# Kernel optimization log

Measured on AMD Instinct MI355X. Metric: run time of the kernel, lower is better.

Reference implementation:

```python
import jax, jax.numpy as jnp
import numpy as np

EPS = 1e-16


def _grads4(x):
    """Four directional shift-differences with zero 'same' padding.

    Matches the fixed 3x3 depthwise conv kernels (cross-correlation):
      Gy: x[i-1,j]   - x[i+1,j]
      Gx: x[i,j-1]   - x[i,j+1]
      GD: x[i-1,j-1] - x[i+1,j+1]
      Gd: x[i-1,j+1] - x[i+1,j-1]
    x: [B, C, H, W]
    """
    B, C, H, W = x.shape
    xp = jnp.pad(x, ((0, 0), (0, 0), (1, 1), (1, 1)))  # zero pad like padding='same'
    gy = xp[:, :, 0:H,     1:W + 1] - xp[:, :, 2:H + 2, 1:W + 1]
    gx = xp[:, :, 1:H + 1, 0:W]     - xp[:, :, 1:H + 1, 2:W + 2]
    gD = xp[:, :, 0:H,     0:W]     - xp[:, :, 2:H + 2, 2:W + 2]
    gd = xp[:, :, 0:H,     2:W + 2] - xp[:, :, 2:H + 2, 0:W]
    return jnp.concatenate([gy, gx, gD, gd], axis=1)  # [B, 4C, H, W]


def setup_inputs() -> dict:
    key = jax.random.key(0)
    k1, k2 = jax.random.split(key)
    shape = (16, 6, 512, 512)
    outputs = jax.random.normal(k1, shape, dtype=jnp.float32)
    labels = jax.random.normal(k2, shape, dtype=jnp.float32)
    return {"outputs": outputs, "labels": labels}


def reference(outputs, labels):
    g_out = _grads4(outputs)
    g_lab = _grads4(labels)
    l1 = jnp.mean(jnp.abs(g_out - g_lab))
    return jnp.sqrt(l1 + EPS)
```

## Files before the change

### kernel.cpp

```cpp
#include <hip/hip_runtime.h>
#include <math.h>


#define NTHREADS 256
#define TROWS 16
#define SROWS (TROWS + 2)
#define WV 512
#define HT 512
#define PLANES 96
#define STRIPS (HT / TROWS)
#define NBLOCKS (PLANES * STRIPS)
#define F4_PER_TILE (SROWS * WV / 4)
#define LD_PER_THREAD (F4_PER_TILE / NTHREADS)

struct Row { float d[8]; float eL, eR; };

__device__ __forceinline__ Row lds_row(const float* __restrict__ sd,
                                       int sr, int lane) {
    Row row;
    const float4 a = *reinterpret_cast<const float4*>(sd + sr * WV + lane * 8);
    const float4 b = *reinterpret_cast<const float4*>(sd + sr * WV + lane * 8 + 4);
    row.d[0] = a.x; row.d[1] = a.y; row.d[2] = a.z; row.d[3] = a.w;
    row.d[4] = b.x; row.d[5] = b.y; row.d[6] = b.z; row.d[7] = b.w;
    const float up = __shfl_up(row.d[7], 1, 64);
    const float dn = __shfl_down(row.d[0], 1, 64);
    row.eL = (lane == 0)  ? 0.f : up;
    row.eR = (lane == 63) ? 0.f : dn;
    return row;
}

__global__ __launch_bounds__(NTHREADS, 4) void struct_loss_partial(
        const float* __restrict__ out_p, const float* __restrict__ lab_p,
        float* __restrict__ partials) {
    __shared__ float sd[SROWS * WV];

    const int plane = blockIdx.x >> 5;
    const int strip = blockIdx.x & (STRIPS - 1);
    const int row0  = strip * TROWS;
    const size_t pbase = (size_t)plane * (HT * WV);

    float4 ov[LD_PER_THREAD], lv[LD_PER_THREAD];
    #pragma unroll
    for (int k = 0; k < LD_PER_THREAD; ++k) {
        const int p  = threadIdx.x + NTHREADS * k;
        const int r  = p >> 7;
        const int c4 = p & 127;
        const int gr = row0 + r - 1;
        const int grc = min(max(gr, 0), HT - 1);
        const size_t goff = pbase + (size_t)grc * WV + c4 * 4;
        ov[k] = *reinterpret_cast<const float4*>(out_p + goff);
        lv[k] = *reinterpret_cast<const float4*>(lab_p + goff);
    }
    #pragma unroll
    for (int k = 0; k < LD_PER_THREAD; ++k) {
        const int p = threadIdx.x + NTHREADS * k;
        const int r = p >> 7;
        const int gr = row0 + r - 1;
        const float m = (gr >= 0 && gr < HT) ? 1.f : 0.f;
        float4 d;
        d.x = m * (ov[k].x - lv[k].x);
        d.y = m * (ov[k].y - lv[k].y);
        d.z = m * (ov[k].z - lv[k].z);
        d.w = m * (ov[k].w - lv[k].w);
        *reinterpret_cast<float4*>(sd + (size_t)p * 4) = d;
    }
    __syncthreads();

    const int wv   = threadIdx.x >> 6;
    const int lane = threadIdx.x & 63;
    float acc = 0.f;

    Row rp = lds_row(sd, wv * 4,     lane);
    Row rc = lds_row(sd, wv * 4 + 1, lane);
    #pragma unroll
    for (int rr = 0; rr < 4; ++rr) {
        Row rn = lds_row(sd, wv * 4 + 2 + rr, lane);

        #pragma unroll
        for (int k = 0; k < 8; ++k) {
            const float cL = (k > 0) ? rc.d[k - 1] : rc.eL;
            const float cR = (k < 7) ? rc.d[k + 1] : rc.eR;
            const float pL = (k > 0) ? rp.d[k - 1] : rp.eL;
            const float pR = (k < 7) ? rp.d[k + 1] : rp.eR;
            const float nL = (k > 0) ? rn.d[k - 1] : rn.eL;
            const float nR = (k < 7) ? rn.d[k + 1] : rn.eR;

            const float gy = rp.d[k] - rn.d[k];
            const float gx = cL - cR;
            const float gD = pL - nR;
            const float gd = pR - nL;
            acc += fabsf(gy) + fabsf(gx) + fabsf(gD) + fabsf(gd);
        }
        rp = rc;
        rc = rn;
    }

    #pragma unroll
    for (int off = 32; off > 0; off >>= 1)
        acc += __shfl_down(acc, off, 64);

    __shared__ float smem[NTHREADS / 64];
    if (lane == 0) smem[wv] = acc;
    __syncthreads();
    if (threadIdx.x == 0) {
        float s = 0.f;
        #pragma unroll
        for (int w = 0; w < NTHREADS / 64; ++w) s += smem[w];
        partials[blockIdx.x] = s;
    }
}

__global__ __launch_bounds__(256) void struct_loss_final(
        const float* __restrict__ partial, float* __restrict__ out,
        int nparts, double inv_count) {
    double acc = 0.0;
    for (int i = threadIdx.x; i < nparts; i += blockDim.x)
        acc += (double)partial[i];
    #pragma unroll
    for (int off = 32; off > 0; off >>= 1)
        acc += __shfl_down(acc, off, 64);
    __shared__ double smem[4];
    const int lane = threadIdx.x & 63;
    const int wid  = threadIdx.x >> 6;
    if (lane == 0) smem[wid] = acc;
    __syncthreads();
    if (threadIdx.x == 0) {
        double s = smem[0] + smem[1] + smem[2] + smem[3];
        out[0] = (float)sqrt(s * inv_count + 1e-16);
    }
}

extern "C" void kernel_launch(void* const* d_in, const int* in_sizes, int n_in,
                              void* d_out, int out_size, void* d_ws, size_t ws_size,
                              hipStream_t stream) {
    const float* outputs = (const float*)d_in[0];
    const float* labels  = (const float*)d_in[1];
    float* out = (float*)d_out;
    float* partials = (float*)d_ws;

    const double inv_count = 1.0 / (16.0 * 24.0 * 512.0 * 512.0);

    struct_loss_partial<<<NBLOCKS, NTHREADS, 0, stream>>>(outputs, labels, partials);
    struct_loss_final<<<1, 256, 0, stream>>>(partials, out, NBLOCKS, inv_count);
}
```

Baseline: 42.17 us.

## Load tiles directly into LDS with global_load_lds and halve strip height

Replaces register-staged global loads with direct global-to-LDS DMA loads of both the outputs and labels tiles. The difference and boundary masking now happen at LDS read time instead of before the store. Strip height drops from 16 to 8 rows, doubling the block count, and the occupancy hint in launch bounds is removed. The intent is to cut VGPR pressure and raise memory-level parallelism, at the cost of more halo re-reads (10/8 instead of 18/16) and twice the LDS footprint per block.

```diff
diff --git a/kernel.cpp b/kernel.cpp
--- a/kernel.cpp
+++ b/kernel.cpp
@@ -3,25 +3,36 @@
 
 
 #define NTHREADS 256
-#define TROWS 16
+#define TROWS 8
 #define SROWS (TROWS + 2)
 #define WV 512
 #define HT 512
 #define PLANES 96
 #define STRIPS (HT / TROWS)
 #define NBLOCKS (PLANES * STRIPS)
-#define F4_PER_TILE (SROWS * WV / 4)
-#define LD_PER_THREAD (F4_PER_TILE / NTHREADS)
+#define TILE_F (SROWS * WV)
+#define CHUNKS (2 * SROWS * 2)
+#define CHUNKS_PER_WAVE (CHUNKS / 4)
+
+__device__ __forceinline__ void gload_lds16(const float* g, float* l) {
+    __builtin_amdgcn_global_load_lds(
+        (const __attribute__((address_space(1))) void*)g,
+        (__attribute__((address_space(3))) void*)l, 16, 0, 0);
+}
 
 struct Row { float d[8]; float eL, eR; };
 
 __device__ __forceinline__ Row lds_row(const float* __restrict__ sd,
-                                       int sr, int lane) {
+                                       int sr, int lane, float m) {
+    const float4 a  = *reinterpret_cast<const float4*>(sd + sr * WV + lane * 8);
+    const float4 b  = *reinterpret_cast<const float4*>(sd + sr * WV + lane * 8 + 4);
+    const float4 c  = *reinterpret_cast<const float4*>(sd + TILE_F + sr * WV + lane * 8);
+    const float4 dd = *reinterpret_cast<const float4*>(sd + TILE_F + sr * WV + lane * 8 + 4);
     Row row;
-    const float4 a = *reinterpret_cast<const float4*>(sd + sr * WV + lane * 8);
-    const float4 b = *reinterpret_cast<const float4*>(sd + sr * WV + lane * 8 + 4);
-    row.d[0] = a.x; row.d[1] = a.y; row.d[2] = a.z; row.d[3] = a.w;
-    row.d[4] = b.x; row.d[5] = b.y; row.d[6] = b.z; row.d[7] = b.w;
+    row.d[0] = m * (a.x - c.x);  row.d[1] = m * (a.y - c.y);
+    row.d[2] = m * (a.z - c.z);  row.d[3] = m * (a.w - c.w);
+    row.d[4] = m * (b.x - dd.x); row.d[5] = m * (b.y - dd.y);
+    row.d[6] = m * (b.z - dd.z); row.d[7] = m * (b.w - dd.w);
     const float up = __shfl_up(row.d[7], 1, 64);
     const float dn = __shfl_down(row.d[0], 1, 64);
     row.eL = (lane == 0)  ? 0.f : up;
@@ -29,70 +40,63 @@
     return row;
 }
 
-__global__ __launch_bounds__(NTHREADS, 4) void struct_loss_partial(
+__global__ __launch_bounds__(NTHREADS) void struct_loss_partial(
         const float* __restrict__ out_p, const float* __restrict__ lab_p,
         float* __restrict__ partials) {
-    __shared__ float sd[SROWS * WV];
+    __shared__ float sd[2 * TILE_F];
 
-    const int plane = blockIdx.x >> 5;
+    const int plane = blockIdx.x >> 6;
     const int strip = blockIdx.x & (STRIPS - 1);
     const int row0  = strip * TROWS;
     const size_t pbase = (size_t)plane * (HT * WV);
 
-    float4 ov[LD_PER_THREAD], lv[LD_PER_THREAD];
+    const int wid  = threadIdx.x >> 6;
+    const int lane = threadIdx.x & 63;
+
     #pragma unroll
-    for (int k = 0; k < LD_PER_THREAD; ++k) {
-        const int p  = threadIdx.x + NTHREADS * k;
-        const int r  = p >> 7;
-        const int c4 = p & 127;
-        const int gr = row0 + r - 1;
-        const int grc = min(max(gr, 0), HT - 1);
-        const size_t goff = pbase + (size_t)grc * WV + c4 * 4;
-        ov[k] = *reinterpret_cast<const float4*>(out_p + goff);
-        lv[k] = *reinterpret_cast<const float4*>(lab_p + goff);
-    }
-    #pragma unroll
-    for (int k = 0; k < LD_PER_THREAD; ++k) {
-        const int p = threadIdx.x + NTHREADS * k;
-        const int r = p >> 7;
-        const int gr = row0 + r - 1;
-        const float m = (gr >= 0 && gr < HT) ? 1.f : 0.f;
-        float4 d;
-        d.x = m * (ov[k].x - lv[k].x);
-        d.y = m * (ov[k].y - lv[k].y);
-        d.z = m * (ov[k].z - lv[k].z);
-        d.w = m * (ov[k].w - lv[k].w);
-        *reinterpret_cast<float4*>(sd + (size_t)p * 4) = d;
+    for (int k = 0; k < CHUNKS_PER_WAVE; ++k) {
+        const int c   = wid * CHUNKS_PER_WAVE + k;
+        const int arr = (c >= CHUNKS / 2) ? 1 : 0;
+        const int cc  = c - (CHUNKS / 2) * arr;
+        const int r   = cc >> 1;
+        const int h   = cc & 1;
+        const int gr  = min(max(row0 + r - 1, 0), HT - 1);
+        const float* src = (arr ? lab_p : out_p) + pbase
+                         + (size_t)gr * WV + h * 256 + lane * 4;
+        gload_lds16(src, sd + c * 256);
     }
     __syncthreads();
 
-    const int wv   = threadIdx.x >> 6;
-    const int lane = threadIdx.x & 63;
     float acc = 0.f;
+    {
+        const int sr0 = wid * 2;
+        const float m0 = ((unsigned)(row0 + sr0 - 1) < (unsigned)HT) ? 1.f : 0.f;
+        Row rp = lds_row(sd, sr0,     lane, m0);
+        Row rc = lds_row(sd, sr0 + 1, lane, 1.f);
+        #pragma unroll
+        for (int rr = 0; rr < 2; ++rr) {
+            const int sr = sr0 + 2 + rr;
+            const float mn = ((unsigned)(row0 + sr - 1) < (unsigned)HT) ? 1.f : 0.f;
+            Row rn = lds_row(sd, sr, lane, mn);
 
-    Row rp = lds_row(sd, wv * 4,     lane);
-    Row rc = lds_row(sd, wv * 4 + 1, lane);
-    #pragma unroll
-    for (int rr = 0; rr < 4; ++rr) {
-        Row rn = lds_row(sd, wv * 4 + 2 + rr, lane);
+            #pragma unroll
+            for (int k = 0; k < 8; ++k) {
+                const float cL = (k > 0) ? rc.d[k - 1] : rc.eL;
+                const float cR = (k < 7) ? rc.d[k + 1] : rc.eR;
+                const float pL = (k > 0) ? rp.d[k - 1] : rp.eL;
+                const float pR = (k < 7) ? rp.d[k + 1] : rp.eR;
+                const float nL = (k > 0) ? rn.d[k - 1] : rn.eL;
+                const float nR = (k < 7) ? rn.d[k + 1] : rn.eR;
 
-        #pragma unroll
-        for (int k = 0; k < 8; ++k) {
-            const float cL = (k > 0) ? rc.d[k - 1] : rc.eL;
-            const float cR = (k < 7) ? rc.d[k + 1] : rc.eR;
-            const float pL = (k > 0) ? rp.d[k - 1] : rp.eL;
-            const float pR = (k < 7) ? rp.d[k + 1] : rp.eR;
-            const float nL = (k > 0) ? rn.d[k - 1] : rn.eL;
-            const float nR = (k < 7) ? rn.d[k + 1] : rn.eR;
-
-            const float gy = rp.d[k] - rn.d[k];
-            const float gx = cL - cR;
-            const float gD = pL - nR;
-            const float gd = pR - nL;
-            acc += fabsf(gy) + fabsf(gx) + fabsf(gD) + fabsf(gd);
+                const float gy = rp.d[k] - rn.d[k];
+                const float gx = cL - cR;
+                const float gD = pL - nR;
+                const float gd = pR - nL;
+                acc += fabsf(gy) + fabsf(gx) + fabsf(gD) + fabsf(gd);
+            }
+            rp = rc;
+            rc = rn;
         }
-        rp = rc;
-        rc = rn;
     }
 
     #pragma unroll
@@ -100,7 +104,7 @@
         acc += __shfl_down(acc, off, 64);
 
     __shared__ float smem[NTHREADS / 64];
-    if (lane == 0) smem[wv] = acc;
+    if (lane == 0) smem[wid] = acc;
     __syncthreads();
     if (threadIdx.x == 0) {
         float s = 0.f;
```

After: 48.10 us. 1.14x slower.

## Process four strips per block with register-prefetched next tile overlapping compute

Applied to the files above, without the earlier changes.

Each block now handles four consecutive strips instead of one, cutting the grid by a factor of four. Global loads for the next strip are issued into registers before the current strip's LDS stencil compute, then written to shared memory after a barrier, so load latency overlaps compute. Sched barriers keep the compiler from sinking the loads, and the occupancy hint in launch bounds is dropped. The trade-off is fewer blocks in flight, higher register pressure from holding the prefetched float4s, and extra barriers per strip.

```diff
diff --git a/kernel.cpp b/kernel.cpp
--- a/kernel.cpp
+++ b/kernel.cpp
@@ -8,10 +8,11 @@
 #define WV 512
 #define HT 512
 #define PLANES 96
-#define STRIPS (HT / TROWS)
-#define NBLOCKS (PLANES * STRIPS)
-#define F4_PER_TILE (SROWS * WV / 4)
-#define LD_PER_THREAD (F4_PER_TILE / NTHREADS)
+#define STRIPS_PER_PLANE (HT / TROWS)
+#define TOTAL_STRIPS (PLANES * STRIPS_PER_PLANE)
+#define SPB 4
+#define NBLOCKS (TOTAL_STRIPS / SPB)
+#define LDK 9
 
 struct Row { float d[8]; float eL, eR; };
 
@@ -29,34 +30,35 @@
     return row;
 }
 
-__global__ __launch_bounds__(NTHREADS, 4) void struct_loss_partial(
-        const float* __restrict__ out_p, const float* __restrict__ lab_p,
-        float* __restrict__ partials) {
-    __shared__ float sd[SROWS * WV];
-
-    const int plane = blockIdx.x >> 5;
-    const int strip = blockIdx.x & (STRIPS - 1);
-    const int row0  = strip * TROWS;
+__device__ __forceinline__ void issue_loads(const float* __restrict__ out_p,
+                                            const float* __restrict__ lab_p,
+                                            int s, int tid,
+                                            float4 (&ov)[LDK], float4 (&lv)[LDK]) {
+    const int plane = s >> 5;
+    const int row0  = (s & 31) * TROWS;
     const size_t pbase = (size_t)plane * (HT * WV);
-
-    float4 ov[LD_PER_THREAD], lv[LD_PER_THREAD];
     #pragma unroll
-    for (int k = 0; k < LD_PER_THREAD; ++k) {
-        const int p  = threadIdx.x + NTHREADS * k;
+    for (int k = 0; k < LDK; ++k) {
+        const int p  = tid + NTHREADS * k;
         const int r  = p >> 7;
         const int c4 = p & 127;
-        const int gr = row0 + r - 1;
-        const int grc = min(max(gr, 0), HT - 1);
-        const size_t goff = pbase + (size_t)grc * WV + c4 * 4;
+        const int gr = min(max(row0 + r - 1, 0), HT - 1);
+        const size_t goff = pbase + (size_t)gr * WV + c4 * 4;
         ov[k] = *reinterpret_cast<const float4*>(out_p + goff);
         lv[k] = *reinterpret_cast<const float4*>(lab_p + goff);
     }
+}
+
+__device__ __forceinline__ void write_tile(float* __restrict__ sd, int s, int tid,
+                                           const float4 (&ov)[LDK],
+                                           const float4 (&lv)[LDK]) {
+    const int row0 = (s & 31) * TROWS;
     #pragma unroll
-    for (int k = 0; k < LD_PER_THREAD; ++k) {
-        const int p = threadIdx.x + NTHREADS * k;
+    for (int k = 0; k < LDK; ++k) {
+        const int p = tid + NTHREADS * k;
         const int r = p >> 7;
         const int gr = row0 + r - 1;
-        const float m = (gr >= 0 && gr < HT) ? 1.f : 0.f;
+        const float m = ((unsigned)gr < (unsigned)HT) ? 1.f : 0.f;
         float4 d;
         d.x = m * (ov[k].x - lv[k].x);
         d.y = m * (ov[k].y - lv[k].y);
@@ -64,18 +66,17 @@
         d.w = m * (ov[k].w - lv[k].w);
         *reinterpret_cast<float4*>(sd + (size_t)p * 4) = d;
     }
-    __syncthreads();
+}
 
-    const int wv   = threadIdx.x >> 6;
-    const int lane = threadIdx.x & 63;
+__device__ __forceinline__ float compute_tile(const float* __restrict__ sd,
+                                              int wid, int lane) {
     float acc = 0.f;
-
-    Row rp = lds_row(sd, wv * 4,     lane);
-    Row rc = lds_row(sd, wv * 4 + 1, lane);
+    const int sr0 = wid * 4;
+    Row rp = lds_row(sd, sr0,     lane);
+    Row rc = lds_row(sd, sr0 + 1, lane);
     #pragma unroll
     for (int rr = 0; rr < 4; ++rr) {
-        Row rn = lds_row(sd, wv * 4 + 2 + rr, lane);
-
+        Row rn = lds_row(sd, sr0 + 2 + rr, lane);
         #pragma unroll
         for (int k = 0; k < 8; ++k) {
             const float cL = (k > 0) ? rc.d[k - 1] : rc.eL;
@@ -94,15 +95,49 @@
         rp = rc;
         rc = rn;
     }
+    return acc;
+}
+
+__global__ __launch_bounds__(NTHREADS) void struct_loss_partial(
+        const float* __restrict__ out_p, const float* __restrict__ lab_p,
+        float* __restrict__ partials) {
+    __shared__ float sd[SROWS * WV];
+
+    const int tid  = threadIdx.x;
+    const int wid  = tid >> 6;
+    const int lane = tid & 63;
+    const int s0   = blockIdx.x * SPB;
+
+    float acc = 0.f;
+    float4 ov[LDK], lv[LDK];
+
+    issue_loads(out_p, lab_p, s0, tid, ov, lv);
+    __builtin_amdgcn_sched_barrier(0);
+    write_tile(sd, s0, tid, ov, lv);
+    __syncthreads();
+
+    #pragma unroll
+    for (int t = 0; t < SPB; ++t) {
+        if (t + 1 < SPB) {
+            issue_loads(out_p, lab_p, s0 + t + 1, tid, ov, lv);
+            __builtin_amdgcn_sched_barrier(0);
+        }
+        acc += compute_tile(sd, wid, lane);
+        __syncthreads();
+        if (t + 1 < SPB) {
+            write_tile(sd, s0 + t + 1, tid, ov, lv);
+            __syncthreads();
+        }
+    }
 
     #pragma unroll
     for (int off = 32; off > 0; off >>= 1)
         acc += __shfl_down(acc, off, 64);
 
     __shared__ float smem[NTHREADS / 64];
-    if (lane == 0) smem[wv] = acc;
+    if (lane == 0) smem[wid] = acc;
     __syncthreads();
-    if (threadIdx.x == 0) {
+    if (tid == 0) {
         float s = 0.f;
         #pragma unroll
         for (int w = 0; w < NTHREADS / 64; ++w) s += smem[w];
```

After: 40.16 us. 4.8% less time.
